# Kernel optimization log

Hardware: AMD Instinct MI355X
Metric: run time of the kernel (lower is better)

## Reference

```python
import jax, jax.numpy as jnp
import numpy as np

BN_EPS = 1e-5


def setup_inputs() -> dict:
    key = jax.random.key(0)
    k1, k2, k3 = jax.random.split(key, 3)
    n, d = 4096, 128
    x = jax.random.normal(k1, (2 * n, d), dtype=jnp.float32)
    affinity_A = jax.random.normal(k2, (n, n), dtype=jnp.float32)
    # Xavier-uniform-like init for the [d, d] weight
    lim = float(np.sqrt(6.0 / (d + d)))
    weight = jax.random.uniform(k3, (d, d), dtype=jnp.float32, minval=-lim, maxval=lim)
    gamma = jnp.ones((d,), dtype=jnp.float32)
    beta = jnp.zeros((d,), dtype=jnp.float32)
    return {"x": x, "affinity_A": affinity_A, "weight": weight, "gamma": gamma, "beta": beta}


def reference(x, affinity_A, weight, gamma, beta):
    # Binarize affinity
    A = jnp.where(affinity_A > 0, 1.0, 0.0).astype(x.dtype)  # [n, n]
    n = A.shape[0]
    I = jnp.eye(n, dtype=x.dtype)
    # Block adjacency [[A, I], [I, A]] -> [2n, 2n]
    adj = jnp.block([[A, I], [I, A]])
    # Symmetric normalization D^{-1/2} A D^{-1/2}.
    # (Original code materializes D^{-1/2} as a full matrix and does two O(n^3)
    # matmuls; mathematically it is just row/column scaling, done here directly.)
    deg = adj.sum(axis=1)                 # [2n], >= 1 because of identity blocks
    dinv = deg ** -0.5
    norm_A = dinv[:, None] * adj * dinv[None, :]
    # GCN propagation: (norm_A @ x) @ W
    h = (norm_A @ x) @ weight             # [2n, d]
    # BatchNorm1d (training mode, biased variance) + ReLU
    mean = h.mean(axis=0)
    var = h.var(axis=0)
    h = (h - mean) * jax.lax.rsqrt(var + BN_EPS) * gamma + beta
    return jax.nn.relu(h)
```

## Files before the change

### kernel.cpp

```cpp
#include <hip/hip_runtime.h>
#include <stdint.h>


#define N_NODES 4096
#define D 128
#define TWO_N (2*N_NODES)

typedef unsigned short u16;
typedef __bf16 bf16;
typedef bf16 bf16x8 __attribute__((ext_vector_type(8)));
typedef float f32x4 __attribute__((ext_vector_type(4)));
typedef u16 u16x8 __attribute__((ext_vector_type(8)));

__device__ __forceinline__ float bf2f(u16 u) {
    return __builtin_bit_cast(float, ((unsigned)u) << 16);
}
__device__ __forceinline__ u16 f2bf(float f) {
    unsigned b = __builtin_bit_cast(unsigned, f);
    unsigned r = (b + 0x7FFFu + ((b >> 16) & 1u)) >> 16;
    return (u16)r;
}
__device__ __forceinline__ bool det_fp32(const u16* gamma) {
    return gamma[0] != (u16)0x3F80;
}

__global__ void k_degscale(const void* __restrict__ x, const void* __restrict__ aff,
                           const void* __restrict__ W, const u16* __restrict__ gamma,
                           float* __restrict__ dinv, u16* __restrict__ XsT,
                           u16* __restrict__ WT) {
    int t = threadIdx.x;
    bool fp32 = det_fp32(gamma);
    const u16* W16 = (const u16*)W;
    const float* W32 = (const float*)W;

    if (blockIdx.x >= 256) {
        int o = (blockIdx.x - 256) * 16 + (t >> 4);
        int cg = (t & 15) * 8;
        u16x8 wv;
        #pragma unroll
        for (int e = 0; e < 8; ++e) {
            size_t wi = (size_t)(cg + e) * D + o;
            float v = fp32 ? W32[wi] : bf2f(W16[wi]);
            wv[e] = f2bf(v);
        }
        *reinterpret_cast<u16x8*>(WT + (size_t)o * D + cg) = wv;
        return;
    }

    __shared__ int scnt[16];
    __shared__ float sdinv[16];
    int wid = t >> 6, lane = t & 63;
    int j0 = blockIdx.x * 16;

    int cnt[4] = {0, 0, 0, 0};
    if (!fp32) {
        const u16* base = (const u16*)aff + (size_t)(j0 + wid * 4) * N_NODES;
        #pragma unroll
        for (int r = 0; r < 4; ++r)
            #pragma unroll
            for (int k = 0; k < 8; ++k) {
                u16x8 v = *reinterpret_cast<const u16x8*>(base + (size_t)r * N_NODES + k * 512 + lane * 8);
                #pragma unroll
                for (int e = 0; e < 8; ++e) cnt[r] += ((short)v[e] > 0) ? 1 : 0;
            }
    } else {
        const float* base = (const float*)aff + (size_t)(j0 + wid * 4) * N_NODES;
        #pragma unroll
        for (int r = 0; r < 4; ++r)
            #pragma unroll
            for (int k = 0; k < 16; ++k) {
                f32x4 v = *reinterpret_cast<const f32x4*>(base + (size_t)r * N_NODES + k * 256 + lane * 4);
                #pragma unroll
                for (int e = 0; e < 4; ++e) cnt[r] += (v[e] > 0.f) ? 1 : 0;
            }
    }
    #pragma unroll
    for (int r = 0; r < 4; ++r) {
        int c = cnt[r];
        #pragma unroll
        for (int off = 32; off; off >>= 1) c += __shfl_down(c, off, 64);
        if (lane == 0) scnt[wid * 4 + r] = c;
    }
    __syncthreads();
    if (t < 16) {
        float d = rsqrtf((float)(scnt[t] + 1));
        sdinv[t] = d;
        dinv[j0 + t] = d;
    }
    __syncthreads();

    int cc = t & 127;
    const u16* xb16 = (const u16*)x + ((t < 128) ? (size_t)0 : (size_t)N_NODES * D);
    const float* xb32 = (const float*)x + ((t < 128) ? (size_t)0 : (size_t)N_NODES * D);
    u16x8 b0, b1;
    #pragma unroll
    for (int jl = 0; jl < 8; ++jl) {
        size_t xi = (size_t)(j0 + jl) * D + cc;
        float xv = fp32 ? xb32[xi] : bf2f(xb16[xi]);
        b0[jl] = f2bf(sdinv[jl] * xv);
    }
    #pragma unroll
    for (int jl = 0; jl < 8; ++jl) {
        size_t xi = (size_t)(j0 + 8 + jl) * D + cc;
        float xv = fp32 ? xb32[xi] : bf2f(xb16[xi]);
        b1[jl] = f2bf(sdinv[8 + jl] * xv);
    }
    *reinterpret_cast<u16x8*>(XsT + (size_t)t * N_NODES + j0) = b0;
    *reinterpret_cast<u16x8*>(XsT + (size_t)t * N_NODES + j0 + 8) = b1;
}

#define BM 32
#define BN 256
#define BK 64
#define SK 4
#define KCHUNK (N_NODES / SK)
#define LDSS 68

__launch_bounds__(256, 2)
__global__ void k_gemm(const void* __restrict__ aff, const u16* __restrict__ XsT,
                       const u16* __restrict__ gamma, u16* __restrict__ Ypart) {
    __shared__ u16 sA[BM * LDSS];
    __shared__ u16 sB[BN * LDSS];
    int tid = threadIdx.x;
    bool fp32 = det_fp32(gamma);
    int mt = blockIdx.x >> 2;
    int sk = blockIdx.x & 3;
    int rm0 = mt * BM;
    int kk0 = sk * KCHUNK;
    int lane = tid & 63, wid = tid >> 6;
    int quad = lane >> 4, l15 = lane & 15;

    f32x4 acc[2][4];
    #pragma unroll
    for (int i = 0; i < 2; ++i)
        #pragma unroll
        for (int j = 0; j < 4; ++j) acc[i][j] = (f32x4){0.f, 0.f, 0.f, 0.f};

    int arow = tid >> 3;
    int acol = (tid & 7) * 8;
    const u16* agp16 = (const u16*)aff + (size_t)(rm0 + arow) * N_NODES + kk0 + acol;
    const float* agp32 = (const float*)aff + (size_t)(rm0 + arow) * N_NODES + kk0 + acol;
    int brow0 = tid >> 3;
    int bcol = (tid & 7) * 8;
    const u16* bgp = XsT + (size_t)brow0 * N_NODES + kk0 + bcol;

    u16x8 pa16; f32x4 pa32a, pa32b;
    u16x8 pb[8];

    if (!fp32) pa16 = *reinterpret_cast<const u16x8*>(agp16);
    else { pa32a = *reinterpret_cast<const f32x4*>(agp32); pa32b = *reinterpret_cast<const f32x4*>(agp32 + 4); }
    #pragma unroll
    for (int p = 0; p < 8; ++p)
        pb[p] = *reinterpret_cast<const u16x8*>(bgp + (size_t)p * 32 * N_NODES);

    for (int kk = 0; kk < KCHUNK / BK; ++kk) {
        u16x8 ab;
        if (!fp32) {
            #pragma unroll
            for (int e = 0; e < 8; ++e) ab[e] = ((short)pa16[e] > 0) ? (u16)0x3F80 : (u16)0;
        } else {
            #pragma unroll
            for (int e = 0; e < 4; ++e) {
                ab[e]     = (pa32a[e] > 0.f) ? (u16)0x3F80 : (u16)0;
                ab[4 + e] = (pa32b[e] > 0.f) ? (u16)0x3F80 : (u16)0;
            }
        }
        __syncthreads();
        *reinterpret_cast<u16x8*>(sA + arow * LDSS + acol) = ab;
        #pragma unroll
        for (int p = 0; p < 8; ++p)
            *reinterpret_cast<u16x8*>(sB + (p * 32 + brow0) * LDSS + bcol) = pb[p];
        __syncthreads();

        if (kk < KCHUNK / BK - 1) {
            int off = (kk + 1) * BK;
            if (!fp32) pa16 = *reinterpret_cast<const u16x8*>(agp16 + off);
            else { pa32a = *reinterpret_cast<const f32x4*>(agp32 + off); pa32b = *reinterpret_cast<const f32x4*>(agp32 + off + 4); }
            #pragma unroll
            for (int p = 0; p < 8; ++p)
                pb[p] = *reinterpret_cast<const u16x8*>(bgp + (size_t)p * 32 * N_NODES + off);
        }

        #pragma unroll
        for (int ks = 0; ks < 2; ++ks) {
            bf16x8 af0 = *reinterpret_cast<const bf16x8*>(sA + l15 * LDSS + ks * 32 + quad * 8);
            bf16x8 af1 = *reinterpret_cast<const bf16x8*>(sA + (16 + l15) * LDSS + ks * 32 + quad * 8);
            #pragma unroll
            for (int j = 0; j < 4; ++j) {
                bf16x8 bfr = *reinterpret_cast<const bf16x8*>(sB + (wid * 64 + j * 16 + l15) * LDSS + ks * 32 + quad * 8);
                acc[0][j] = __builtin_amdgcn_mfma_f32_16x16x32_bf16(af0, bfr, acc[0][j], 0, 0, 0);
                acc[1][j] = __builtin_amdgcn_mfma_f32_16x16x32_bf16(af1, bfr, acc[1][j], 0, 0, 0);
            }
        }
    }

    u16* yp = Ypart + (size_t)sk * N_NODES * 256;
    #pragma unroll
    for (int i = 0; i < 2; ++i) {
        int row = rm0 + i * 16 + quad * 4;
        #pragma unroll
        for (int j = 0; j < 4; ++j) {
            int col = wid * 64 + j * 16 + l15;
            #pragma unroll
            for (int r = 0; r < 4; ++r)
                yp[(size_t)(row + r) * 256 + col] = f2bf(acc[i][j][r]);
        }
    }
}

__global__ void k_comb(const u16* __restrict__ Ypart, const void* __restrict__ x,
                       const u16* __restrict__ WT, const u16* __restrict__ gamma,
                       const float* __restrict__ dinv, u16* __restrict__ hpre,
                       float* __restrict__ pS, float* __restrict__ pQ) {
    __shared__ u16 sH[32 * 136];
    __shared__ u16 sWT[128 * 136];
    __shared__ float sOut[32 * 132];
    int t = threadIdx.x;
    bool fp32 = det_fp32(gamma);
    int r0 = blockIdx.x * 32;
    bool top = blockIdx.x < 128;
    int node0 = top ? r0 : r0 - N_NODES;
    const u16* x16 = (const u16*)x;
    const float* x32 = (const float*)x;

    #pragma unroll
    for (int p = 0; p < 2; ++p) {
        int r = (t >> 4) + p * 16;
        int c0 = (t & 15) * 8;
        int node = node0 + r;
        int ycol = (top ? 0 : 128) + c0;
        float fs[8] = {0.f, 0.f, 0.f, 0.f, 0.f, 0.f, 0.f, 0.f};
        #pragma unroll
        for (int sk = 0; sk < SK; ++sk) {
            u16x8 yv = *reinterpret_cast<const u16x8*>(Ypart + ((size_t)sk * N_NODES + node) * 256 + ycol);
            #pragma unroll
            for (int e = 0; e < 8; ++e) fs[e] += bf2f(yv[e]);
        }
        float dv = dinv[node];
        size_t xi = (top ? (size_t)(N_NODES + node) : (size_t)node) * D + c0;
        u16x8 hv;
        if (!fp32) {
            u16x8 xv = *reinterpret_cast<const u16x8*>(x16 + xi);
            #pragma unroll
            for (int e = 0; e < 8; ++e) hv[e] = f2bf(dv * fs[e] + dv * dv * bf2f(xv[e]));
        } else {
            f32x4 xa = *reinterpret_cast<const f32x4*>(x32 + xi);
            f32x4 xb = *reinterpret_cast<const f32x4*>(x32 + xi + 4);
            #pragma unroll
            for (int e = 0; e < 4; ++e) {
                hv[e]     = f2bf(dv * fs[e]     + dv * dv * xa[e]);
                hv[4 + e] = f2bf(dv * fs[4 + e] + dv * dv * xb[e]);
            }
        }
        *reinterpret_cast<u16x8*>(sH + r * 136 + c0) = hv;
    }
    #pragma unroll
    for (int p = 0; p < 8; ++p) {
        int idx = p * 256 + t;
        int o = idx >> 4;
        int cg = (idx & 15) * 8;
        u16x8 wv = *reinterpret_cast<const u16x8*>(WT + (size_t)o * D + cg);
        *reinterpret_cast<u16x8*>(sWT + o * 136 + cg) = wv;
    }
    __syncthreads();

    int lane = t & 63, wid = t >> 6;
    int wm = wid >> 1, wn = wid & 1;
    int quad = lane >> 4, l15 = lane & 15;
    f32x4 acc[4];
    #pragma unroll
    for (int j = 0; j < 4; ++j) acc[j] = (f32x4){0.f, 0.f, 0.f, 0.f};
    #pragma unroll
    for (int ks = 0; ks < 4; ++ks) {
        bf16x8 af = *reinterpret_cast<const bf16x8*>(sH + (wm * 16 + l15) * 136 + ks * 32 + quad * 8);
        #pragma unroll
        for (int j = 0; j < 4; ++j) {
            bf16x8 bfr = *reinterpret_cast<const bf16x8*>(sWT + (wn * 64 + j * 16 + l15) * 136 + ks * 32 + quad * 8);
            acc[j] = __builtin_amdgcn_mfma_f32_16x16x32_bf16(af, bfr, acc[j], 0, 0, 0);
        }
    }
    #pragma unroll
    for (int j = 0; j < 4; ++j) {
        int row = wm * 16 + quad * 4;
        int col = wn * 64 + j * 16 + l15;
        #pragma unroll
        for (int r = 0; r < 4; ++r) sOut[(row + r) * 132 + col] = acc[j][r];
    }
    __syncthreads();
    #pragma unroll
    for (int p = 0; p < 16; ++p) {
        int idx = p * 256 + t;
        int r = idx >> 7, c = idx & 127;
        hpre[(size_t)(r0 + r) * D + c] = f2bf(sOut[r * 132 + c]);
    }
    if (t < 128) {
        float s = 0.f, q = 0.f;
        #pragma unroll
        for (int r = 0; r < 32; ++r) {
            float v = sOut[r * 132 + t];
            s += v; q += v * v;
        }
        pS[blockIdx.x * 128 + t] = s;
        pQ[blockIdx.x * 128 + t] = q;
    }
}

__global__ void k_stats(const float* __restrict__ pS, const float* __restrict__ pQ,
                        const void* __restrict__ gamma, const void* __restrict__ beta,
                        const u16* __restrict__ gdet, float* __restrict__ scsh) {
    __shared__ float rs[256], rq[256];
    int t = threadIdx.x;
    int c0 = blockIdx.x * 8;
    int cl = t & 7;
    int rr = t >> 3;
    float s = 0.f, q = 0.f;
    #pragma unroll
    for (int i = 0; i < 8; ++i) {
        int row = rr + i * 32;
        s += pS[row * 128 + c0 + cl];
        q += pQ[row * 128 + c0 + cl];
    }
    rs[t] = s; rq[t] = q;
    __syncthreads();
    #pragma unroll
    for (int st = 128; st >= 8; st >>= 1) {
        if (t < st) { rs[t] += rs[t + st]; rq[t] += rq[t + st]; }
        __syncthreads();
    }
    if (t < 8) {
        bool fp32 = det_fp32(gdet);
        int c = c0 + t;
        float mean = rs[t] * (1.0f / TWO_N);
        float var = fmaxf(rq[t] * (1.0f / TWO_N) - mean * mean, 0.f);
        float inv = rsqrtf(var + 1e-5f);
        float g = fp32 ? ((const float*)gamma)[c] : bf2f(((const u16*)gamma)[c]);
        float b = fp32 ? ((const float*)beta)[c]  : bf2f(((const u16*)beta)[c]);
        scsh[c] = inv * g;
        scsh[128 + c] = b - mean * inv * g;
    }
}

__global__ void k_bn(const u16* __restrict__ hpre, const float* __restrict__ scsh,
                     const u16* __restrict__ gdet, void* __restrict__ out) {
    __shared__ float ssc[128], ssh[128];
    int t = threadIdx.x;
    bool fp32 = det_fp32(gdet);
    if (t < 128) { ssc[t] = scsh[t]; ssh[t] = scsh[128 + t]; }
    __syncthreads();
    size_t base = (size_t)blockIdx.x * 2048 + t * 8;
    int c0 = (t & 15) * 8;
    u16x8 hv = *reinterpret_cast<const u16x8*>(hpre + base);
    if (!fp32) {
        u16x8 ov;
        #pragma unroll
        for (int e = 0; e < 8; ++e) {
            float v = bf2f(hv[e]) * ssc[c0 + e] + ssh[c0 + e];
            ov[e] = f2bf(fmaxf(v, 0.f));
        }
        *reinterpret_cast<u16x8*>((u16*)out + base) = ov;
    } else {
        float* o = (float*)out + base;
        #pragma unroll
        for (int e = 0; e < 8; ++e) {
            float v = bf2f(hv[e]) * ssc[c0 + e] + ssh[c0 + e];
            o[e] = fmaxf(v, 0.f);
        }
    }
}

extern "C" void kernel_launch(void* const* d_in, const int* in_sizes, int n_in,
                              void* d_out, int out_size, void* d_ws, size_t ws_size,
                              hipStream_t stream) {
    const void* x = d_in[0];
    const void* aff = d_in[1];
    const void* W = d_in[2];
    const u16* gamma = (const u16*)d_in[3];
    const void* beta = d_in[4];

    char* ws = (char*)d_ws;
    u16* XsT = (u16*)ws;
    u16* hpre = XsT;
    u16* Ypart = (u16*)(ws + 2097152);
    float* dinv = (float*)(ws + 10485760);
    float* pS = (float*)(ws + 10502144);
    float* pQ = (float*)(ws + 10633216);
    float* scsh = (float*)(ws + 10764288);
    u16* WT = (u16*)(ws + 10765312);

    k_degscale<<<264, 256, 0, stream>>>(x, aff, W, gamma, dinv, XsT, WT);
    k_gemm<<<512, 256, 0, stream>>>(aff, XsT, gamma, Ypart);
    k_comb<<<256, 256, 0, stream>>>(Ypart, x, WT, gamma, dinv, hpre, pS, pQ);
    k_stats<<<16, 256, 0, stream>>>(pS, pQ, gamma, beta, gamma, scsh);
    k_bn<<<512, 256, 0, stream>>>(hpre, scsh, gamma, d_out);
}
```

Measured before the change: 137.0 us.

## Bit-pack binarized affinity in degree pass and stream packed bits into GEMM

The degree kernel now binarizes the affinity matrix into a bitmask (one byte per 8 entries) while counting degrees, and transposes the scaled x through shared memory. The main GEMM reads this packed bitmask instead of the full fp32/bf16 affinity matrix, expands the bits to bf16 ones in registers, and feeds MFMA directly from global memory without LDS staging, using 64-row tiles and split-K of 8. The affinity matrix is read from memory only once instead of twice, in exchange for extra Ypart partial traffic and the loss of shared-memory reuse for the B operand. The combine kernel is retiled to 16 rows per block to match.

```diff
diff --git a/kernel.cpp b/kernel.cpp
--- a/kernel.cpp
+++ b/kernel.cpp
@@ -27,14 +27,14 @@
 __global__ void k_degscale(const void* __restrict__ x, const void* __restrict__ aff,
                            const void* __restrict__ W, const u16* __restrict__ gamma,
                            float* __restrict__ dinv, u16* __restrict__ XsT,
-                           u16* __restrict__ WT) {
+                           u16* __restrict__ WT, unsigned char* __restrict__ pack) {
     int t = threadIdx.x;
     bool fp32 = det_fp32(gamma);
-    const u16* W16 = (const u16*)W;
-    const float* W32 = (const float*)W;
-
-    if (blockIdx.x >= 256) {
-        int o = (blockIdx.x - 256) * 16 + (t >> 4);
+
+    if (blockIdx.x >= 512) {
+        const u16* W16 = (const u16*)W;
+        const float* W32 = (const float*)W;
+        int o = (blockIdx.x - 512) * 16 + (t >> 4);
         int cg = (t & 15) * 8;
         u16x8 wv;
         #pragma unroll
@@ -47,160 +47,144 @@
         return;
     }
 
-    __shared__ int scnt[16];
-    __shared__ float sdinv[16];
+    __shared__ int scnt[8];
+    __shared__ float sdinv[8];
+    __shared__ u16 sx[16 * 136];
     int wid = t >> 6, lane = t & 63;
-    int j0 = blockIdx.x * 16;
-
-    int cnt[4] = {0, 0, 0, 0};
-    if (!fp32) {
-        const u16* base = (const u16*)aff + (size_t)(j0 + wid * 4) * N_NODES;
-        #pragma unroll
-        for (int r = 0; r < 4; ++r)
-            #pragma unroll
-            for (int k = 0; k < 8; ++k) {
-                u16x8 v = *reinterpret_cast<const u16x8*>(base + (size_t)r * N_NODES + k * 512 + lane * 8);
+    int j0 = blockIdx.x * 8;
+
+    #pragma unroll
+    for (int r = 0; r < 2; ++r) {
+        int row = j0 + wid * 2 + r;
+        int cnt = 0;
+        #pragma unroll
+        for (int k = 0; k < 8; ++k) {
+            unsigned by = 0;
+            if (!fp32) {
+                u16x8 v = *reinterpret_cast<const u16x8*>((const u16*)aff + (size_t)row * N_NODES + k * 512 + lane * 8);
                 #pragma unroll
-                for (int e = 0; e < 8; ++e) cnt[r] += ((short)v[e] > 0) ? 1 : 0;
+                for (int e = 0; e < 8; ++e) by |= (((short)v[e] > 0) ? 1u : 0u) << e;
+            } else {
+                f32x4 v0 = *reinterpret_cast<const f32x4*>((const float*)aff + (size_t)row * N_NODES + k * 512 + lane * 8);
+                f32x4 v1 = *reinterpret_cast<const f32x4*>((const float*)aff + (size_t)row * N_NODES + k * 512 + lane * 8 + 4);
+                #pragma unroll
+                for (int e = 0; e < 4; ++e) {
+                    by |= ((v0[e] > 0.f) ? 1u : 0u) << e;
+                    by |= ((v1[e] > 0.f) ? 1u : 0u) << (4 + e);
+                }
             }
-    } else {
-        const float* base = (const float*)aff + (size_t)(j0 + wid * 4) * N_NODES;
-        #pragma unroll
-        for (int r = 0; r < 4; ++r)
-            #pragma unroll
-            for (int k = 0; k < 16; ++k) {
-                f32x4 v = *reinterpret_cast<const f32x4*>(base + (size_t)r * N_NODES + k * 256 + lane * 4);
-                #pragma unroll
-                for (int e = 0; e < 4; ++e) cnt[r] += (v[e] > 0.f) ? 1 : 0;
-            }
-    }
-    #pragma unroll
-    for (int r = 0; r < 4; ++r) {
-        int c = cnt[r];
-        #pragma unroll
-        for (int off = 32; off; off >>= 1) c += __shfl_down(c, off, 64);
-        if (lane == 0) scnt[wid * 4 + r] = c;
-    }
-    __syncthreads();
-    if (t < 16) {
+            pack[(size_t)row * 512 + k * 64 + lane] = (unsigned char)by;
+            cnt += __popc(by);
+        }
+        #pragma unroll
+        for (int off = 32; off; off >>= 1) cnt += __shfl_down(cnt, off, 64);
+        if (lane == 0) scnt[wid * 2 + r] = cnt;
+    }
+    __syncthreads();
+    if (t < 8) {
         float d = rsqrtf((float)(scnt[t] + 1));
         sdinv[t] = d;
         dinv[j0 + t] = d;
     }
     __syncthreads();
 
-    int cc = t & 127;
-    const u16* xb16 = (const u16*)x + ((t < 128) ? (size_t)0 : (size_t)N_NODES * D);
-    const float* xb32 = (const float*)x + ((t < 128) ? (size_t)0 : (size_t)N_NODES * D);
-    u16x8 b0, b1;
-    #pragma unroll
-    for (int jl = 0; jl < 8; ++jl) {
-        size_t xi = (size_t)(j0 + jl) * D + cc;
-        float xv = fp32 ? xb32[xi] : bf2f(xb16[xi]);
-        b0[jl] = f2bf(sdinv[jl] * xv);
-    }
-    #pragma unroll
-    for (int jl = 0; jl < 8; ++jl) {
-        size_t xi = (size_t)(j0 + 8 + jl) * D + cc;
-        float xv = fp32 ? xb32[xi] : bf2f(xb16[xi]);
-        b1[jl] = f2bf(sdinv[8 + jl] * xv);
-    }
-    *reinterpret_cast<u16x8*>(XsT + (size_t)t * N_NODES + j0) = b0;
-    *reinterpret_cast<u16x8*>(XsT + (size_t)t * N_NODES + j0 + 8) = b1;
-}
-
-#define BM 32
-#define BN 256
-#define BK 64
-#define SK 4
+    {
+        int rr = t >> 4;
+        int c0 = (t & 15) * 8;
+        size_t grow = (rr < 8) ? (size_t)(j0 + rr) : (size_t)(N_NODES + j0 + rr - 8);
+        float dv = sdinv[rr & 7];
+        u16x8 o;
+        if (!fp32) {
+            u16x8 xv = *reinterpret_cast<const u16x8*>((const u16*)x + grow * D + c0);
+            #pragma unroll
+            for (int e = 0; e < 8; ++e) o[e] = f2bf(dv * bf2f(xv[e]));
+        } else {
+            f32x4 xa = *reinterpret_cast<const f32x4*>((const float*)x + grow * D + c0);
+            f32x4 xb = *reinterpret_cast<const f32x4*>((const float*)x + grow * D + c0 + 4);
+            #pragma unroll
+            for (int e = 0; e < 4; ++e) {
+                o[e] = f2bf(dv * xa[e]);
+                o[4 + e] = f2bf(dv * xb[e]);
+            }
+        }
+        *reinterpret_cast<u16x8*>(sx + rr * 136 + c0) = o;
+    }
+    __syncthreads();
+
+    {
+        int c = t;
+        int rbase = (c < 128) ? 0 : 8;
+        int cl = c & 127;
+        u16x8 o;
+        #pragma unroll
+        for (int jl = 0; jl < 8; ++jl) o[jl] = sx[(rbase + jl) * 136 + cl];
+        *reinterpret_cast<u16x8*>(XsT + (size_t)c * N_NODES + j0) = o;
+    }
+}
+
+#define SK 8
 #define KCHUNK (N_NODES / SK)
-#define LDSS 68
 
 __launch_bounds__(256, 2)
-__global__ void k_gemm(const void* __restrict__ aff, const u16* __restrict__ XsT,
-                       const u16* __restrict__ gamma, u16* __restrict__ Ypart) {
-    __shared__ u16 sA[BM * LDSS];
-    __shared__ u16 sB[BN * LDSS];
+__global__ void k_gemm(const uint32_t* __restrict__ pack32, const u16* __restrict__ XsT,
+                       u16* __restrict__ Ypart) {
     int tid = threadIdx.x;
-    bool fp32 = det_fp32(gamma);
-    int mt = blockIdx.x >> 2;
-    int sk = blockIdx.x & 3;
-    int rm0 = mt * BM;
-    int kk0 = sk * KCHUNK;
+    int mt = blockIdx.x >> 3;
+    int sk = blockIdx.x & 7;
+    int r0 = mt * 64;
+    int k0 = sk * KCHUNK;
     int lane = tid & 63, wid = tid >> 6;
     int quad = lane >> 4, l15 = lane & 15;
-
-    f32x4 acc[2][4];
-    #pragma unroll
-    for (int i = 0; i < 2; ++i)
+    int c0 = wid * 64;
+    int shift = quad * 8;
+
+    f32x4 acc[4][4];
+    #pragma unroll
+    for (int i = 0; i < 4; ++i)
         #pragma unroll
         for (int j = 0; j < 4; ++j) acc[i][j] = (f32x4){0.f, 0.f, 0.f, 0.f};
 
-    int arow = tid >> 3;
-    int acol = (tid & 7) * 8;
-    const u16* agp16 = (const u16*)aff + (size_t)(rm0 + arow) * N_NODES + kk0 + acol;
-    const float* agp32 = (const float*)aff + (size_t)(rm0 + arow) * N_NODES + kk0 + acol;
-    int brow0 = tid >> 3;
-    int bcol = (tid & 7) * 8;
-    const u16* bgp = XsT + (size_t)brow0 * N_NODES + kk0 + bcol;
-
-    u16x8 pa16; f32x4 pa32a, pa32b;
-    u16x8 pb[8];
-
-    if (!fp32) pa16 = *reinterpret_cast<const u16x8*>(agp16);
-    else { pa32a = *reinterpret_cast<const f32x4*>(agp32); pa32b = *reinterpret_cast<const f32x4*>(agp32 + 4); }
-    #pragma unroll
-    for (int p = 0; p < 8; ++p)
-        pb[p] = *reinterpret_cast<const u16x8*>(bgp + (size_t)p * 32 * N_NODES);
-
-    for (int kk = 0; kk < KCHUNK / BK; ++kk) {
-        u16x8 ab;
-        if (!fp32) {
-            #pragma unroll
-            for (int e = 0; e < 8; ++e) ab[e] = ((short)pa16[e] > 0) ? (u16)0x3F80 : (u16)0;
-        } else {
-            #pragma unroll
-            for (int e = 0; e < 4; ++e) {
-                ab[e]     = (pa32a[e] > 0.f) ? (u16)0x3F80 : (u16)0;
-                ab[4 + e] = (pa32b[e] > 0.f) ? (u16)0x3F80 : (u16)0;
-            }
-        }
-        __syncthreads();
-        *reinterpret_cast<u16x8*>(sA + arow * LDSS + acol) = ab;
-        #pragma unroll
-        for (int p = 0; p < 8; ++p)
-            *reinterpret_cast<u16x8*>(sB + (p * 32 + brow0) * LDSS + bcol) = pb[p];
-        __syncthreads();
-
-        if (kk < KCHUNK / BK - 1) {
-            int off = (kk + 1) * BK;
-            if (!fp32) pa16 = *reinterpret_cast<const u16x8*>(agp16 + off);
-            else { pa32a = *reinterpret_cast<const f32x4*>(agp32 + off); pa32b = *reinterpret_cast<const f32x4*>(agp32 + off + 4); }
-            #pragma unroll
-            for (int p = 0; p < 8; ++p)
-                pb[p] = *reinterpret_cast<const u16x8*>(bgp + (size_t)p * 32 * N_NODES + off);
-        }
-
-        #pragma unroll
-        for (int ks = 0; ks < 2; ++ks) {
-            bf16x8 af0 = *reinterpret_cast<const bf16x8*>(sA + l15 * LDSS + ks * 32 + quad * 8);
-            bf16x8 af1 = *reinterpret_cast<const bf16x8*>(sA + (16 + l15) * LDSS + ks * 32 + quad * 8);
-            #pragma unroll
-            for (int j = 0; j < 4; ++j) {
-                bf16x8 bfr = *reinterpret_cast<const bf16x8*>(sB + (wid * 64 + j * 16 + l15) * LDSS + ks * 32 + quad * 8);
-                acc[0][j] = __builtin_amdgcn_mfma_f32_16x16x32_bf16(af0, bfr, acc[0][j], 0, 0, 0);
-                acc[1][j] = __builtin_amdgcn_mfma_f32_16x16x32_bf16(af1, bfr, acc[1][j], 0, 0, 0);
-            }
-        }
+    const u16* bp[4];
+    #pragma unroll
+    for (int j = 0; j < 4; ++j)
+        bp[j] = XsT + (size_t)(c0 + j * 16 + l15) * N_NODES + k0 + quad * 8;
+    const uint32_t* ap[4];
+    #pragma unroll
+    for (int i = 0; i < 4; ++i)
+        ap[i] = pack32 + (size_t)(r0 + i * 16 + l15) * 128 + (k0 >> 5);
+
+    for (int s = 0; s < KCHUNK / 32; ++s) {
+        u16x8 bv[4];
+        uint32_t ad[4];
+        #pragma unroll
+        for (int j = 0; j < 4; ++j) { bv[j] = *reinterpret_cast<const u16x8*>(bp[j]); bp[j] += 32; }
+        #pragma unroll
+        for (int i = 0; i < 4; ++i) { ad[i] = *ap[i]; ap[i] += 1; }
+
+        bf16x8 af[4];
+        #pragma unroll
+        for (int i = 0; i < 4; ++i) {
+            unsigned by = (ad[i] >> shift) & 0xFFu;
+            u16x8 e;
+            #pragma unroll
+            for (int e2 = 0; e2 < 8; ++e2)
+                e[e2] = ((by >> e2) & 1u) ? (u16)0x3F80 : (u16)0;
+            af[i] = __builtin_bit_cast(bf16x8, e);
+        }
+        #pragma unroll
+        for (int i = 0; i < 4; ++i)
+            #pragma unroll
+            for (int j = 0; j < 4; ++j)
+                acc[i][j] = __builtin_amdgcn_mfma_f32_16x16x32_bf16(af[i], __builtin_bit_cast(bf16x8, bv[j]), acc[i][j], 0, 0, 0);
     }
 
     u16* yp = Ypart + (size_t)sk * N_NODES * 256;
     #pragma unroll
-    for (int i = 0; i < 2; ++i) {
-        int row = rm0 + i * 16 + quad * 4;
+    for (int i = 0; i < 4; ++i) {
+        int row = r0 + i * 16 + quad * 4;
         #pragma unroll
         for (int j = 0; j < 4; ++j) {
-            int col = wid * 64 + j * 16 + l15;
+            int col = c0 + j * 16 + l15;
             #pragma unroll
             for (int r = 0; r < 4; ++r)
                 yp[(size_t)(row + r) * 256 + col] = f2bf(acc[i][j][r]);
@@ -212,20 +196,19 @@
                        const u16* __restrict__ WT, const u16* __restrict__ gamma,
                        const float* __restrict__ dinv, u16* __restrict__ hpre,
                        float* __restrict__ pS, float* __restrict__ pQ) {
-    __shared__ u16 sH[32 * 136];
+    __shared__ u16 sH[16 * 136];
     __shared__ u16 sWT[128 * 136];
-    __shared__ float sOut[32 * 132];
+    __shared__ float sOut[16 * 132];
     int t = threadIdx.x;
     bool fp32 = det_fp32(gamma);
-    int r0 = blockIdx.x * 32;
-    bool top = blockIdx.x < 128;
+    int r0 = blockIdx.x * 16;
+    bool top = blockIdx.x < 256;
     int node0 = top ? r0 : r0 - N_NODES;
     const u16* x16 = (const u16*)x;
     const float* x32 = (const float*)x;
 
-    #pragma unroll
-    for (int p = 0; p < 2; ++p) {
-        int r = (t >> 4) + p * 16;
+    {
+        int r = t >> 4;
         int c0 = (t & 15) * 8;
         int node = node0 + r;
         int ycol = (top ? 0 : 128) + c0;
@@ -265,30 +248,29 @@
     __syncthreads();
 
     int lane = t & 63, wid = t >> 6;
-    int wm = wid >> 1, wn = wid & 1;
     int quad = lane >> 4, l15 = lane & 15;
-    f32x4 acc[4];
-    #pragma unroll
-    for (int j = 0; j < 4; ++j) acc[j] = (f32x4){0.f, 0.f, 0.f, 0.f};
+    f32x4 acc[2];
+    acc[0] = (f32x4){0.f, 0.f, 0.f, 0.f};
+    acc[1] = (f32x4){0.f, 0.f, 0.f, 0.f};
     #pragma unroll
     for (int ks = 0; ks < 4; ++ks) {
-        bf16x8 af = *reinterpret_cast<const bf16x8*>(sH + (wm * 16 + l15) * 136 + ks * 32 + quad * 8);
-        #pragma unroll
-        for (int j = 0; j < 4; ++j) {
-            bf16x8 bfr = *reinterpret_cast<const bf16x8*>(sWT + (wn * 64 + j * 16 + l15) * 136 + ks * 32 + quad * 8);
+        bf16x8 af = *reinterpret_cast<const bf16x8*>(sH + l15 * 136 + ks * 32 + quad * 8);
+        #pragma unroll
+        for (int j = 0; j < 2; ++j) {
+            bf16x8 bfr = *reinterpret_cast<const bf16x8*>(sWT + (wid * 32 + j * 16 + l15) * 136 + ks * 32 + quad * 8);
             acc[j] = __builtin_amdgcn_mfma_f32_16x16x32_bf16(af, bfr, acc[j], 0, 0, 0);
         }
     }
     #pragma unroll
-    for (int j = 0; j < 4; ++j) {
-        int row = wm * 16 + quad * 4;
-        int col = wn * 64 + j * 16 + l15;
+    for (int j = 0; j < 2; ++j) {
+        int row = quad * 4;
+        int col = wid * 32 + j * 16 + l15;
         #pragma unroll
         for (int r = 0; r < 4; ++r) sOut[(row + r) * 132 + col] = acc[j][r];
     }
     __syncthreads();
     #pragma unroll
-    for (int p = 0; p < 16; ++p) {
+    for (int p = 0; p < 8; ++p) {
         int idx = p * 256 + t;
         int r = idx >> 7, c = idx & 127;
         hpre[(size_t)(r0 + r) * D + c] = f2bf(sOut[r * 132 + c]);
@@ -296,7 +278,7 @@
     if (t < 128) {
         float s = 0.f, q = 0.f;
         #pragma unroll
-        for (int r = 0; r < 32; ++r) {
+        for (int r = 0; r < 16; ++r) {
             float v = sOut[r * 132 + t];
             s += v; q += v * v;
         }
@@ -315,7 +297,7 @@
     int rr = t >> 3;
     float s = 0.f, q = 0.f;
     #pragma unroll
-    for (int i = 0; i < 8; ++i) {
+    for (int i = 0; i < 16; ++i) {
         int row = rr + i * 32;
         s += pS[row * 128 + c0 + cl];
         q += pQ[row * 128 + c0 + cl];
@@ -381,15 +363,16 @@
     u16* XsT = (u16*)ws;
     u16* hpre = XsT;
     u16* Ypart = (u16*)(ws + 2097152);
-    float* dinv = (float*)(ws + 10485760);
-    float* pS = (float*)(ws + 10502144);
-    float* pQ = (float*)(ws + 10633216);
-    float* scsh = (float*)(ws + 10764288);
-    u16* WT = (u16*)(ws + 10765312);
-
-    k_degscale<<<264, 256, 0, stream>>>(x, aff, W, gamma, dinv, XsT, WT);
-    k_gemm<<<512, 256, 0, stream>>>(aff, XsT, gamma, Ypart);
-    k_comb<<<256, 256, 0, stream>>>(Ypart, x, WT, gamma, dinv, hpre, pS, pQ);
+    unsigned char* pack = (unsigned char*)(ws + 18874368);
+    float* dinv = (float*)(ws + 20971520);
+    float* pS = (float*)(ws + 20987904);
+    float* pQ = (float*)(ws + 21250048);
+    float* scsh = (float*)(ws + 21512192);
+    u16* WT = (u16*)(ws + 21513216);
+
+    k_degscale<<<520, 256, 0, stream>>>(x, aff, W, gamma, dinv, XsT, WT, pack);
+    k_gemm<<<512, 256, 0, stream>>>((const uint32_t*)pack, XsT, Ypart);
+    k_comb<<<512, 256, 0, stream>>>(Ypart, x, WT, gamma, dinv, hpre, pS, pQ);
     k_stats<<<16, 256, 0, stream>>>(pS, pQ, gamma, beta, gamma, scsh);
     k_bn<<<512, 256, 0, stream>>>(hpre, scsh, gamma, d_out);
 }
```

Measured after the change: 154.9 us. 1.13x slower.
